# Optimization experiments

Hardware: AMD Instinct MI355X
Metric: run time of the kernel (lower is better)

## Reference

```python
import jax, jax.numpy as jnp
import numpy as np

EPS = 1e-5

def _conv(x, w, pad):
    return jax.lax.conv_general_dilated(
        x, w, window_strides=(1, 1), padding=[(pad, pad), (pad, pad)],
        dimension_numbers=('NCHW', 'OIHW', 'NCHW'))

def _bn(x, g, b):
    # training-mode batch norm over (N, H, W), matching nn.BatchNorm2d in train mode
    m = x.mean(axis=(0, 2, 3), keepdims=True)
    v = x.var(axis=(0, 2, 3), keepdims=True)
    return (x - m) * jax.lax.rsqrt(v + EPS) * g[None, :, None, None] + b[None, :, None, None]

def setup_inputs() -> dict:
    key = jax.random.key(0)
    ks = jax.random.split(key, 16)
    B, C, H, W = 64, 16, 128, 128
    f32 = jnp.float32
    x = jax.random.normal(ks[0], (B, C, H, W), dtype=f32)
    # conv weights (OIHW), He-ish scale
    conv_w1 = jax.random.normal(ks[1], (32, 16, 1, 1), f32) * (2.0 / 16) ** 0.5
    conv_w2 = jax.random.normal(ks[2], (64, 32, 1, 1), f32) * (2.0 / 32) ** 0.5
    conv_w3 = jax.random.normal(ks[3], (32, 64, 3, 3), f32) * (2.0 / (64 * 9)) ** 0.5
    conv_w4 = jax.random.normal(ks[4], (32, 32, 3, 3), f32) * (2.0 / (32 * 9)) ** 0.5
    bn1_g = jnp.ones((32,), f32); bn1_b = jnp.zeros((32,), f32)
    bn2_g = jnp.ones((64,), f32); bn2_b = jnp.zeros((64,), f32)
    bn3_g = jnp.ones((32,), f32); bn3_b = jnp.zeros((32,), f32)
    bn4_g = jnp.ones((32,), f32); bn4_b = jnp.zeros((32,), f32)
    fc1_w = jax.random.normal(ks[5], (32, 32), f32) * (1.0 / 32) ** 0.5
    fc1_b = jnp.zeros((32,), f32)
    fc2_w = jax.random.normal(ks[6], (16, 32), f32) * (1.0 / 32) ** 0.5
    fc2_b = jnp.zeros((16,), f32)
    return dict(x=x, conv_w1=conv_w1, bn1_g=bn1_g, bn1_b=bn1_b,
                conv_w2=conv_w2, bn2_g=bn2_g, bn2_b=bn2_b,
                conv_w3=conv_w3, bn3_g=bn3_g, bn3_b=bn3_b,
                conv_w4=conv_w4, bn4_g=bn4_g, bn4_b=bn4_b,
                fc1_w=fc1_w, fc1_b=fc1_b, fc2_w=fc2_w, fc2_b=fc2_b)

def reference(x, conv_w1, bn1_g, bn1_b, conv_w2, bn2_g, bn2_b,
              conv_w3, bn3_g, bn3_b, conv_w4, bn4_g, bn4_b,
              fc1_w, fc1_b, fc2_w, fc2_b):
    B, C, H, W = x.shape  # C == 16
    # spectral: 1x1 convs
    h = jax.nn.relu(_bn(_conv(x, conv_w1, 0), bn1_g, bn1_b))
    h = jax.nn.relu(_bn(_conv(h, conv_w2, 0), bn2_g, bn2_b))
    # spatial: 3x3 convs
    h = jax.nn.relu(_bn(_conv(h, conv_w3, 1), bn3_g, bn3_b))
    x2 = jax.nn.relu(_bn(_conv(h, conv_w4, 1), bn4_g, bn4_b))  # [B,32,H,W]
    tok = x2.reshape(B, 32, H * W).transpose(0, 2, 1)  # [B,HW,32]
    h1 = jnp.tanh(tok @ fc1_w.T + fc1_b)
    w0 = jnp.tanh(h1 @ fc2_w.T + fc2_b)  # [B,HW,16]
    # y0 is computed BEFORE the torch in-place diag zeroing, which never
    # affects any returned value (w0 is unused afterwards) -> omitted.
    y0 = w0.mean(axis=1)  # [B,16]
    Cm = jnp.einsum('bi,bj->bij', y0, y0)  # [B,16,16]
    wn = jnp.linalg.norm(Cm, axis=2)  # [B,16]
    order = jnp.argsort(-wn, axis=-1)  # descending sort indices
    vals = jnp.take_along_axis(wn, order, axis=-1)  # sorted values
    idx = order[:, :15]  # 5 groups of 3 channels
    gath = jnp.take_along_axis(x, idx[:, :, None, None], axis=1)  # [B,15,H,W]
    fi = gath.reshape(B, 5, 3, H, W).transpose(1, 0, 2, 3, 4)  # [5,B,3,H,W]
    wi = vals[:, :15].reshape(B, 5, 3).mean(axis=-1).T  # [5,B]
    cgh = jnp.einsum('bij,bjn->bin', Cm, x.reshape(B, C, H * W))  # [B,16,HW]
    return (fi, wi, vals, order, cgh)
```

## Files before the change

### kernel.cpp

```cpp
#include <hip/hip_runtime.h>

#define TPB 256

static constexpr int   HWc  = 16384;
static constexpr float NINV = 1.0f / 1048576.0f;

static constexpr unsigned FI_OFF    = 0u;
static constexpr unsigned WI_OFF    = 15728640u;
static constexpr unsigned VALS_OFF  = 15728960u;
static constexpr unsigned ORDER_OFF = 15729984u;
static constexpr unsigned CGH_OFF   = 15731008u;

typedef _Float16 f16;
typedef f16   f16x8 __attribute__((ext_vector_type(8)));
typedef f16   f16x4 __attribute__((ext_vector_type(4)));
typedef float f32x4 __attribute__((ext_vector_type(4)));

__device__ __forceinline__ void gl_lds16(const void* g, void* l) {
    __builtin_amdgcn_global_load_lds(
        (const __attribute__((address_space(1))) unsigned int*)g,
        (__attribute__((address_space(3))) unsigned int*)l, 16, 0, 0);
}

__device__ __forceinline__ float wave_sum(float v) {
#pragma unroll
    for (int o = 1; o < 64; o <<= 1) v += __shfl_xor(v, o, 64);
    return v;
}

__device__ __forceinline__ float tanh_fast(float x) {
    float e = __expf(x + x);
    return 1.0f - __fdividef(2.0f, e + 1.0f);
}

__global__ __launch_bounds__(TPB) void k_gramx(const float* __restrict__ x,
                                               float* __restrict__ bkt) {
    __shared__ float red[4][272];
    int tid = threadIdx.x, lane = tid & 63, w = tid >> 6;
    int p = lane & 15, g = lane >> 4;
    const f16 one = (f16)1.0f;
    const f16x8 kOnes = {one, one, one, one, one, one, one, one};
    f32x4 accG = {0.f, 0.f, 0.f, 0.f};
    f32x4 accS = {0.f, 0.f, 0.f, 0.f};
    unsigned wgid = blockIdx.x * 4u + (unsigned)w;
    for (unsigned c = wgid; c < 32768u; c += 2048u) {
        unsigned P0 = c * 32u;
        unsigned b = P0 >> 14, off = P0 & 16383u;
        const float* src = x + ((size_t)b * 16 + p) * HWc + off + g * 8;
        float4 a4 = *(const float4*)src;
        float4 b4 = *(const float4*)(src + 4);
        f16x8 f = { (f16)a4.x, (f16)a4.y, (f16)a4.z, (f16)a4.w,
                    (f16)b4.x, (f16)b4.y, (f16)b4.z, (f16)b4.w };
        accG = __builtin_amdgcn_mfma_f32_16x16x32_f16(f, f, accG, 0, 0, 0);
        accS = __builtin_amdgcn_mfma_f32_16x16x32_f16(kOnes, f, accS, 0, 0, 0);
    }
#pragma unroll
    for (int r = 0; r < 4; ++r) red[w][(4 * g + r) * 16 + p] = accG[r];
    if (g == 0) red[w][256 + p] = accS[0];
    __syncthreads();
    for (int e = tid; e < 272; e += TPB) {
        float v = red[0][e] + red[1][e] + red[2][e] + red[3][e];
        atomicAdd(&bkt[(blockIdx.x & 63u) * 272u + (unsigned)e], v);
    }
}

__global__ void k_sfin1g(const float* __restrict__ bkt, const float* __restrict__ w1,
                         const float* __restrict__ g1, const float* __restrict__ bb1,
                         float* __restrict__ prm) {
    __shared__ float G[256];
    __shared__ float S[16];
    int tid = threadIdx.x;
    {
        float v = 0.f;
        for (int s = 0; s < 64; ++s) v += bkt[s * 272 + tid];
        G[tid] = v;
    }
    if (tid < 16) {
        float v = 0.f;
        for (int s = 0; s < 64; ++s) v += bkt[s * 272 + 256 + tid];
        S[tid] = v;
    }
    __syncthreads();
    if (tid < 32) {
        float wv[16];
#pragma unroll
        for (int i = 0; i < 16; ++i) wv[i] = w1[tid * 16 + i];
        float m = 0.f, e2 = 0.f;
#pragma unroll
        for (int i = 0; i < 16; ++i) {
            m += wv[i] * S[i];
            float t = 0.f;
#pragma unroll
            for (int j = 0; j < 16; ++j) t += wv[j] * G[i * 16 + j];
            e2 += wv[i] * t;
        }
        float mean = m * NINV;
        float var = e2 * NINV - mean * mean;
        float sc = g1[tid] * rsqrtf(var + 1e-5f);
        prm[tid * 2] = sc;
        prm[tid * 2 + 1] = bb1[tid] - mean * sc;
    }
}

__global__ __launch_bounds__(TPB) void k_conv2m(const float* __restrict__ x,
                                                const float* __restrict__ w1,
                                                const float* __restrict__ w2,
                                                const float* __restrict__ prm1,
                                                f16* __restrict__ t2r,
                                                float* __restrict__ bkt) {
    __shared__ __align__(16) float w1s[512];
    __shared__ float p1[64];
    __shared__ __align__(16) f16 V[256 * 40];
    __shared__ float red[4][800];
    int tid = threadIdx.x, lane = tid & 63, w = tid >> 6;
    int p = lane & 15, g = lane >> 4;
    for (int e = tid; e < 512; e += TPB) w1s[e] = w1[e];
    if (tid < 64) p1[tid] = prm1[tid];
    f16x8 Wf[4];
#pragma unroll
    for (int cb = 0; cb < 4; ++cb) {
        const float* wr = w2 + (cb * 16 + p) * 32 + g * 8;
        float4 a4 = *(const float4*)wr;
        float4 b4 = *(const float4*)(wr + 4);
        Wf[cb] = (f16x8){ (f16)a4.x, (f16)a4.y, (f16)a4.z, (f16)a4.w,
                          (f16)b4.x, (f16)b4.y, (f16)b4.z, (f16)b4.w };
    }
    __syncthreads();
    unsigned pid = blockIdx.x * TPB + tid;
    const float* xp = x + (size_t)(pid >> 14) * 16 * HWc + (pid & 16383u);
    float xv[16];
#pragma unroll
    for (int c = 0; c < 16; ++c) xv[c] = xp[(size_t)c * HWc];
    f16* vp = V + tid * 40;
#pragma unroll
    for (int c8 = 0; c8 < 4; ++c8) {
        f16x8 hv;
#pragma unroll
        for (int j = 0; j < 8; ++j) {
            int co = c8 * 8 + j;
            float a = 0.f;
#pragma unroll
            for (int c4 = 0; c4 < 4; ++c4) {
                float4 ww = *(const float4*)&w1s[co * 16 + c4 * 4];
                a = fmaf(xv[c4 * 4 + 0], ww.x, a); a = fmaf(xv[c4 * 4 + 1], ww.y, a);
                a = fmaf(xv[c4 * 4 + 2], ww.z, a); a = fmaf(xv[c4 * 4 + 3], ww.w, a);
            }
            hv[j] = (f16)fmaxf(0.f, fmaf(a, p1[co * 2], p1[co * 2 + 1]));
        }
        *(f16x8*)(vp + c8 * 8) = hv;
    }
    __syncthreads();
    unsigned Pb = blockIdx.x * TPB + (unsigned)(w * 64);
#pragma unroll
    for (int f = 0; f < 4; ++f) {
        int pxl = w * 64 + f * 16 + p;
        f16x8 bf = *(const f16x8*)&V[pxl * 40 + g * 8];
        unsigned Pg = Pb + (unsigned)(f * 16 + p);
#pragma unroll
        for (int cb = 0; cb < 4; ++cb) {
            f32x4 d = {0.f, 0.f, 0.f, 0.f};
            d = __builtin_amdgcn_mfma_f32_16x16x32_f16(Wf[cb], bf, d, 0, 0, 0);
            f16x4 o4 = { (f16)d[0], (f16)d[1], (f16)d[2], (f16)d[3] };
            *(f16x4*)(t2r + (size_t)Pg * 64 + cb * 16 + 4 * g) = o4;
        }
    }
    const f16 one = (f16)1.0f;
    const f16x8 kOnes = {one, one, one, one, one, one, one, one};
    f32x4 accG[3] = {{0.f,0.f,0.f,0.f},{0.f,0.f,0.f,0.f},{0.f,0.f,0.f,0.f}};
    f32x4 accS[2] = {{0.f,0.f,0.f,0.f},{0.f,0.f,0.f,0.f}};
#pragma unroll
    for (int c2 = 0; c2 < 2; ++c2) {
        int px0 = w * 64 + c2 * 32;
        f16x8 fb[2];
#pragma unroll
        for (int cb2 = 0; cb2 < 2; ++cb2)
#pragma unroll
            for (int j = 0; j < 8; ++j)
                fb[cb2][j] = V[(px0 + g * 8 + j) * 40 + cb2 * 16 + p];
        accG[0] = __builtin_amdgcn_mfma_f32_16x16x32_f16(fb[0], fb[0], accG[0], 0, 0, 0);
        accG[1] = __builtin_amdgcn_mfma_f32_16x16x32_f16(fb[0], fb[1], accG[1], 0, 0, 0);
        accG[2] = __builtin_amdgcn_mfma_f32_16x16x32_f16(fb[1], fb[1], accG[2], 0, 0, 0);
        accS[0] = __builtin_amdgcn_mfma_f32_16x16x32_f16(kOnes, fb[0], accS[0], 0, 0, 0);
        accS[1] = __builtin_amdgcn_mfma_f32_16x16x32_f16(kOnes, fb[1], accS[1], 0, 0, 0);
    }
#pragma unroll
    for (int blk = 0; blk < 3; ++blk)
#pragma unroll
        for (int r = 0; r < 4; ++r)
            red[w][blk * 256 + (4 * g + r) * 16 + p] = accG[blk][r];
    if (g == 0) { red[w][768 + p] = accS[0][0]; red[w][784 + p] = accS[1][0]; }
    __syncthreads();
    for (int e = tid; e < 800; e += TPB) {
        float v = red[0][e] + red[1][e] + red[2][e] + red[3][e];
        atomicAdd(&bkt[(blockIdx.x & 63u) * 800u + (unsigned)e], v);
    }
}

__global__ void k_sfin2g(const float* __restrict__ bkt, const float* __restrict__ w2,
                         const float* __restrict__ g2, const float* __restrict__ bb2,
                         float* __restrict__ prm) {
    __shared__ float G[768];
    __shared__ float S[32];
    int tid = threadIdx.x;
    for (int e = tid; e < 768; e += 256) {
        float v = 0.f;
        for (int s = 0; s < 64; ++s) v += bkt[s * 800 + e];
        G[e] = v;
    }
    if (tid < 32) {
        float v = 0.f;
        for (int s = 0; s < 64; ++s) v += bkt[s * 800 + 768 + tid];
        S[tid] = v;
    }
    __syncthreads();
    if (tid < 64) {
        float wv[32];
#pragma unroll
        for (int i = 0; i < 32; ++i) wv[i] = (float)(f16)w2[tid * 32 + i];
        float m = 0.f, e2 = 0.f;
#pragma unroll
        for (int i = 0; i < 32; ++i) {
            m += wv[i] * S[i];
            int bi = i >> 4, il = i & 15;
            float t = 0.f;
#pragma unroll
            for (int j = 0; j < 32; ++j) {
                int bj = j >> 4, jl = j & 15;
                float Gij;
                if (bi <= bj) Gij = G[(bi == 0 ? (bj == 0 ? 0 : 1) : 2) * 256 + il * 16 + jl];
                else          Gij = G[(bj == 0 ? 1 : 2) * 256 + jl * 16 + il];
                t += wv[j] * Gij;
            }
            e2 += wv[i] * t;
        }
        float mean = m * NINV;
        float var = e2 * NINV - mean * mean;
        float sc = g2[tid] * rsqrtf(var + 1e-5f);
        prm[tid * 2] = sc;
        prm[tid * 2 + 1] = bb2[tid] - mean * sc;
    }
}

__global__ void k_sfin(const float* __restrict__ bkt, const float* __restrict__ g,
                       const float* __restrict__ bb, float* __restrict__ prm, int C) {
    int co = threadIdx.x;
    float s = 0.f, q = 0.f;
    for (int k = 0; k < 64; ++k) { s += bkt[(k * C + co) * 2]; q += bkt[(k * C + co) * 2 + 1]; }
    float mean = s * NINV;
    float var = q * NINV - mean * mean;
    float sc = g[co] * rsqrtf(var + 1e-5f);
    prm[co * 2] = sc;
    prm[co * 2 + 1] = bb[co] - mean * sc;
}

template <int CI>
__global__ void k_wprep(const float* __restrict__ w, float* __restrict__ wsg) {
    constexpr int KS = CI / 32;
    int t = blockIdx.x * 256 + threadIdx.x;
    if (t >= KS * 18 * 64) return;
    int lane = t & 63, fr = t >> 6;
    int cf = fr & 1, tap = (fr >> 1) % 9, ks = fr / 18;
    int g = lane >> 4, p = lane & 15;
    int co = cf * 16 + p;
    f16x8 hv;
#pragma unroll
    for (int j = 0; j < 8; ++j) {
        int ci = ks * 32 + g * 8 + j;
        hv[j] = (f16)w[(co * CI + ci) * 9 + tap];
    }
    ((f16x8*)wsg)[fr * 64 + lane] = hv;
}

template <int CI>
__global__ __launch_bounds__(512, 4) void k_conv3(const f16* __restrict__ in,
                                                  const float* __restrict__ wsg,
                                                  const float* __restrict__ prm,
                                                  f16* __restrict__ outp,
                                                  float* __restrict__ bkt) {
    constexpr int KS = CI / 32;
    __shared__ __align__(16) struct {
        f16   Wl[18 * 512];
        f16   Al[6 * 128 * 32];
        float red[8][64];
    } sh;
    int tid = threadIdx.x;
    int lane = tid & 63, w = tid >> 6;
    int p = lane & 15, g = lane >> 4;
    int rw = w >> 1, h = w & 1;
    int cw = tid & 3, pxt = tid >> 2;

    unsigned o = blockIdx.x;
    unsigned xcd = o & 7u, q = o >> 3;
    unsigned rg = q & 31u, grp = q >> 5;
    unsigned b = (grp << 3) | xcd;
    int y0 = (int)rg * 4;

    float psc[KS][8], psh[KS][8];
#pragma unroll
    for (int ks = 0; ks < KS; ++ks)
#pragma unroll
        for (int j = 0; j < 8; ++j) {
            int ch = ks * 32 + cw * 8 + j;
            psc[ks][j] = prm[ch * 2];
            psh[ks][j] = prm[ch * 2 + 1];
        }

    bool mask0 = (h == 0 && p == 0);
    bool mask1 = (h == 1 && p == 15);
    const f16x8 kZ = {0, 0, 0, 0, 0, 0, 0, 0};

    f32x4 acc[4][2];
#pragma unroll
    for (int f = 0; f < 4; ++f)
#pragma unroll
        for (int cf = 0; cf < 2; ++cf) acc[f][cf] = (f32x4){0.f, 0.f, 0.f, 0.f};

    for (int ks = 0; ks < KS; ++ks) {
        if (ks) __syncthreads();
#pragma unroll
        for (int c0 = 0; c0 < 1152; c0 += 512) {
            if (c0 + (w << 6) < 1152) {
                int c = c0 + tid;
                gl_lds16(wsg + (size_t)(ks * 4608 + c * 4), &sh.Wl[c * 8]);
            }
        }
#pragma unroll
        for (int r6 = 0; r6 < 6; ++r6) {
            int yy = y0 - 1 + r6;
            f16* dst = &sh.Al[r6 * 4096 + tid * 8];
            if ((unsigned)yy < 128u) {
                const f16* s = in + ((size_t)(b * 128u + (unsigned)yy) * 128u + pxt) * CI
                                  + ks * 32 + cw * 8;
                f16x8 raw = *(const f16x8*)s;
                f16x8 o8;
#pragma unroll
                for (int j = 0; j < 8; ++j)
                    o8[j] = (f16)fmaxf(0.f, fmaf((float)raw[j], psc[ks][j], psh[ks][j]));
                *(f16x8*)dst = o8;
            } else {
                *(f16x8*)dst = kZ;
            }
        }
        __syncthreads();
        const f16x8* Wv = (const f16x8*)sh.Wl;
        for (int dyi = 0; dyi < 3; ++dyi) {
            int ar = rw + dyi;
#pragma unroll
            for (int dxi = 0; dxi < 3; ++dxi) {
                int tap = dyi * 3 + dxi;
                f16x8 b0 = Wv[(tap * 2 + 0) * 64 + lane];
                f16x8 b1 = Wv[(tap * 2 + 1) * 64 + lane];
#pragma unroll
                for (int f = 0; f < 4; ++f) {
                    int px = h * 64 + f * 16 + p + dxi - 1;
                    f16x8 a = *(const f16x8*)&sh.Al[(ar * 128 + px) * 32 + g * 8];
                    if (dxi == 0 && f == 0) { if (mask0) a = kZ; }
                    if (dxi == 2 && f == 3) { if (mask1) a = kZ; }
                    acc[f][0] = __builtin_amdgcn_mfma_f32_16x16x32_f16(b0, a, acc[f][0], 0, 0, 0);
                    acc[f][1] = __builtin_amdgcn_mfma_f32_16x16x32_f16(b1, a, acc[f][1], 0, 0, 0);
                }
            }
        }
    }

    float sv[8], qv[8];
#pragma unroll
    for (int cf = 0; cf < 2; ++cf)
#pragma unroll
        for (int r = 0; r < 4; ++r) {
            float s = acc[0][cf][r] + acc[1][cf][r] + acc[2][cf][r] + acc[3][cf][r];
            float qq = acc[0][cf][r] * acc[0][cf][r] + acc[1][cf][r] * acc[1][cf][r] +
                       acc[2][cf][r] * acc[2][cf][r] + acc[3][cf][r] * acc[3][cf][r];
#pragma unroll
            for (int m = 1; m < 16; m <<= 1) {
                s += __shfl_xor(s, m, 64);
                qq += __shfl_xor(qq, m, 64);
            }
            sv[cf * 4 + r] = s; qv[cf * 4 + r] = qq;
        }
    if (p == 0) {
#pragma unroll
        for (int cf = 0; cf < 2; ++cf)
#pragma unroll
            for (int r = 0; r < 4; ++r) {
                int co = cf * 16 + g * 4 + r;
                sh.red[w][co * 2] = sv[cf * 4 + r];
                sh.red[w][co * 2 + 1] = qv[cf * 4 + r];
            }
    }

    unsigned pxb = b * 16384u + (unsigned)((y0 + rw) * 128 + h * 64 + p);
#pragma unroll
    for (int f = 0; f < 4; ++f)
#pragma unroll
        for (int cf = 0; cf < 2; ++cf) {
            f16x4 o4 = { (f16)acc[f][cf][0], (f16)acc[f][cf][1],
                         (f16)acc[f][cf][2], (f16)acc[f][cf][3] };
            *(f16x4*)(outp + (size_t)(pxb + f * 16u) * 32u + (unsigned)(cf * 16 + g * 4)) = o4;
        }

    __syncthreads();
    if (tid < 64) {
        float v = 0.f;
#pragma unroll
        for (int ww = 0; ww < 8; ++ww) v += sh.red[ww][tid];
        atomicAdd(&bkt[(o & 63u) * 64u + (unsigned)tid], v);
    }
}

__global__ __launch_bounds__(TPB) void k_fcm(const f16* __restrict__ t4,
                                             const float* __restrict__ prm4,
                                             const float* __restrict__ fw1,
                                             const float* __restrict__ fb1,
                                             const float* __restrict__ fw2,
                                             const float* __restrict__ fb2,
                                             float* __restrict__ y0sum) {
    __shared__ __align__(16) struct {
        f16   V1[256 * 40];
        f16   V2[256 * 40];
        float p4[64], b1s[32], b2s[16];
        float red[4][16];
    } sh;
    int tid = threadIdx.x, lane = tid & 63, w = tid >> 6;
    int p = lane & 15, g = lane >> 4;
    if (tid < 64) sh.p4[tid] = prm4[tid];
    if (tid < 32) sh.b1s[tid] = fb1[tid];
    if (tid < 16) sh.b2s[tid] = fb2[tid];
    f16x8 W1h[2], W1l[2], W2h, W2l;
#pragma unroll
    for (int cb = 0; cb < 2; ++cb) {
        const float* wr = fw1 + (cb * 16 + p) * 32 + g * 8;
#pragma unroll
        for (int j = 0; j < 8; ++j) {
            float v = wr[j];
            f16 hh = (f16)v;
            W1h[cb][j] = hh;
            W1l[cb][j] = (f16)(v - (float)hh);
        }
    }
    {
        const float* wr = fw2 + p * 32 + g * 8;
#pragma unroll
        for (int j = 0; j < 8; ++j) {
            float v = wr[j];
            f16 hh = (f16)v;
            W2h[j] = hh;
            W2l[j] = (f16)(v - (float)hh);
        }
    }
    __syncthreads();
    unsigned pid = blockIdx.x * TPB + tid;
    const f16x8* tv = (const f16x8*)(t4 + (size_t)pid * 32);
    f16* vp = sh.V1 + tid * 40;
#pragma unroll
    for (int c8 = 0; c8 < 4; ++c8) {
        f16x8 raw = tv[c8];
        f16x8 o8;
#pragma unroll
        for (int j = 0; j < 8; ++j) {
            int c = c8 * 8 + j;
            o8[j] = (f16)fmaxf(0.f, fmaf((float)raw[j], sh.p4[c * 2], sh.p4[c * 2 + 1]));
        }
        *(f16x8*)(vp + c8 * 8) = o8;
    }
    __syncthreads();
    float bb1[8];
#pragma unroll
    for (int cb = 0; cb < 2; ++cb)
#pragma unroll
        for (int r = 0; r < 4; ++r) bb1[cb * 4 + r] = sh.b1s[cb * 16 + g * 4 + r];
#pragma unroll
    for (int f = 0; f < 4; ++f) {
        int pxl = w * 64 + f * 16 + p;
        f16x8 bf = *(const f16x8*)&sh.V1[pxl * 40 + g * 8];
#pragma unroll
        for (int cb = 0; cb < 2; ++cb) {
            f32x4 d = {0.f, 0.f, 0.f, 0.f};
            d = __builtin_amdgcn_mfma_f32_16x16x32_f16(W1l[cb], bf, d, 0, 0, 0);
            d = __builtin_amdgcn_mfma_f32_16x16x32_f16(W1h[cb], bf, d, 0, 0, 0);
            f16x4 h4;
#pragma unroll
            for (int r = 0; r < 4; ++r) h4[r] = (f16)tanh_fast(d[r] + bb1[cb * 4 + r]);
            *(f16x4*)&sh.V2[pxl * 40 + cb * 16 + g * 4] = h4;
        }
    }
    __syncthreads();
    float bb2[4];
#pragma unroll
    for (int r = 0; r < 4; ++r) bb2[r] = sh.b2s[g * 4 + r];
    float s4[4] = {0.f, 0.f, 0.f, 0.f};
#pragma unroll
    for (int f = 0; f < 4; ++f) {
        int pxl = w * 64 + f * 16 + p;
        f16x8 bf = *(const f16x8*)&sh.V2[pxl * 40 + g * 8];
        f32x4 d = {0.f, 0.f, 0.f, 0.f};
        d = __builtin_amdgcn_mfma_f32_16x16x32_f16(W2l, bf, d, 0, 0, 0);
        d = __builtin_amdgcn_mfma_f32_16x16x32_f16(W2h, bf, d, 0, 0, 0);
#pragma unroll
        for (int r = 0; r < 4; ++r) s4[r] += tanh_fast(d[r] + bb2[r]);
    }
#pragma unroll
    for (int r = 0; r < 4; ++r) {
#pragma unroll
        for (int m = 1; m < 16; m <<= 1) s4[r] += __shfl_xor(s4[r], m, 64);
    }
    if (p == 0) {
#pragma unroll
        for (int r = 0; r < 4; ++r) sh.red[w][g * 4 + r] = s4[r];
    }
    __syncthreads();
    if (tid < 16) {
        float s = sh.red[0][tid] + sh.red[1][tid] + sh.red[2][tid] + sh.red[3][tid];
        atomicAdd(&y0sum[(blockIdx.x >> 6) * 16u + tid], s);
    }
}

__global__ void k_final(const float* __restrict__ y0sum, float* __restrict__ out,
                        float* __restrict__ Cm, int* __restrict__ idxb) {
    int b = threadIdx.x;
    float y0[16]; float nrm = 0.f;
#pragma unroll
    for (int i = 0; i < 16; ++i) { y0[i] = y0sum[b * 16 + i] * (1.0f / 16384.0f); nrm += y0[i] * y0[i]; }
    nrm = sqrtf(nrm);
    float wn[16]; int id[16];
#pragma unroll
    for (int i = 0; i < 16; ++i) { wn[i] = fabsf(y0[i]) * nrm; id[i] = i; }
    for (int i = 1; i < 16; ++i) {
        float k = wn[i]; int ii = id[i]; int j = i - 1;
        while (j >= 0 && wn[j] < k) { wn[j + 1] = wn[j]; id[j + 1] = id[j]; --j; }
        wn[j + 1] = k; id[j + 1] = ii;
    }
    for (int i = 0; i < 16; ++i) {
        out[VALS_OFF + b * 16 + i] = wn[i];
        out[ORDER_OFF + b * 16 + i] = (float)id[i];
    }
    for (int g = 0; g < 5; ++g)
        out[WI_OFF + g * 64 + b] = (wn[g * 3] + wn[g * 3 + 1] + wn[g * 3 + 2]) * (1.0f / 3.0f);
    for (int i = 0; i < 16; ++i)
        for (int j = 0; j < 16; ++j) Cm[b * 256 + i * 16 + j] = y0[i] * y0[j];
    for (int s = 0; s < 15; ++s) idxb[b * 15 + s] = id[s];
}

__global__ __launch_bounds__(TPB) void k_out(const float* __restrict__ x,
                                             const float* __restrict__ Cm,
                                             const int* __restrict__ idxb,
                                             float* __restrict__ out) {
    __shared__ float cm[256];
    __shared__ int idl[15];
    int tid = threadIdx.x;
    unsigned b = blockIdx.x >> 6;
    unsigned p = ((blockIdx.x & 63u) << 8) + tid;
    cm[tid] = Cm[b * 256u + tid];
    if (tid < 15) idl[tid] = idxb[b * 15u + tid];
    __syncthreads();
    const float* xp = x + (size_t)b * 16 * HWc + p;
    float xv[16];
#pragma unroll
    for (int j = 0; j < 16; ++j) xv[j] = xp[(size_t)j * HWc];
    float* og = out + CGH_OFF + (size_t)b * 16 * HWc + p;
    for (int i = 0; i < 16; ++i) {
        float a = 0.f;
#pragma unroll
        for (int j = 0; j < 16; ++j) a = fmaf(cm[i * 16 + j], xv[j], a);
        og[(size_t)i * HWc] = a;
    }
#pragma unroll
    for (int s = 0; s < 15; ++s) {
        int ch = idl[s];
        float vv = xp[(size_t)ch * HWc];
        int g = s / 3, r = s - 3 * g;
        out[(size_t)((g * 64 + (int)b) * 3 + r) * HWc + p] = vv;
    }
}

extern "C" void kernel_launch(void* const* d_in, const int* in_sizes, int n_in,
                              void* d_out, int out_size, void* d_ws, size_t ws_size,
                              hipStream_t stream) {
    const float* x    = (const float*)d_in[0];
    const float* w1   = (const float*)d_in[1];
    const float* bn1g = (const float*)d_in[2];  const float* bn1b = (const float*)d_in[3];
    const float* w2   = (const float*)d_in[4];
    const float* bn2g = (const float*)d_in[5];  const float* bn2b = (const float*)d_in[6];
    const float* w3   = (const float*)d_in[7];
    const float* bn3g = (const float*)d_in[8];  const float* bn3b = (const float*)d_in[9];
    const float* w4   = (const float*)d_in[10];
    const float* bn4g = (const float*)d_in[11]; const float* bn4b = (const float*)d_in[12];
    const float* fw1  = (const float*)d_in[13]; const float* fb1  = (const float*)d_in[14];
    const float* fw2  = (const float*)d_in[15]; const float* fb2  = (const float*)d_in[16];
    float* out = (float*)d_out;
    float* wsf = (float*)d_ws;

    f16*   t2r = (f16*)wsf;
    f16*   t3r = (f16*)(wsf + 33554432);
    f16*   t4h = (f16*)(wsf + 50331648);
    float* acc = wsf + 67108864;
    float* b1g = acc;
    float* b2g = acc + 17408;
    float* b3  = acc + 68608;
    float* b4  = acc + 76800;
    float* y0s = acc + 84992;
    float* pr1 = acc + 86016;  float* pr2 = acc + 86080;
    float* pr3 = acc + 86208;  float* pr4 = acc + 86272;
    float* Cm  = acc + 86336;
    int*   idxb = (int*)(acc + 102720);
    float* wsg3 = acc + 103680;
    float* wsg4 = acc + 112896;
    size_t need = (size_t)(67108864 + 117504) * 4;
    if (ws_size < need) return;

    hipMemsetAsync(acc, 0, 86016 * 4, stream);

    k_wprep<64><<<9, 256, 0, stream>>>(w3, wsg3);
    k_wprep<32><<<5, 256, 0, stream>>>(w4, wsg4);
    k_gramx<<<512, TPB, 0, stream>>>(x, b1g);
    k_sfin1g<<<1, 256, 0, stream>>>(b1g, w1, bn1g, bn1b, pr1);
    k_conv2m<<<4096, TPB, 0, stream>>>(x, w1, w2, pr1, t2r, b2g);
    k_sfin2g<<<1, 256, 0, stream>>>(b2g, w2, bn2g, bn2b, pr2);
    k_conv3<64><<<2048, 512, 0, stream>>>(t2r, wsg3, pr2, t3r, b3);
    k_sfin<<<1, 32, 0, stream>>>(b3, bn3g, bn3b, pr3, 32);
    k_conv3<32><<<2048, 512, 0, stream>>>(t3r, wsg4, pr3, t4h, b4);
    k_sfin<<<1, 32, 0, stream>>>(b4, bn4g, bn4b, pr4, 32);
    k_fcm<<<4096, TPB, 0, stream>>>(t4h, pr4, fw1, fb1, fw2, fb2, y0s);
    k_final<<<1, 64, 0, stream>>>(y0s, out, Cm, idxb);
    k_out<<<4096, TPB, 0, stream>>>(x, Cm, idxb, out);
}
```

Measured before the change: 365.6 us.

## Fold BN scale into downstream conv/FC weights, apply shift+ReLU in packed f16

The per-channel batch-norm scale is folded into the next layer's weights, so relu(x*sc+sh) becomes sc*relu(x + sh/sc). The activation prologue in the conv3 and fcm kernels shrinks to a packed f16 add and max, with no float conversion and FMA per element. The weight-prep kernels now run after each stats-finalize kernel because they need the scale. This is only valid when the scale is positive (gamma > 0). It also adds f16 rounding of sh/sc and more kernel ordering dependencies.

```diff
diff --git a/kernel.cpp b/kernel.cpp
--- a/kernel.cpp
+++ b/kernel.cpp
@@ -254,7 +254,8 @@
 }
 
 template <int CI>
-__global__ void k_wprep(const float* __restrict__ w, float* __restrict__ wsg) {
+__global__ void k_wprep(const float* __restrict__ w, const float* __restrict__ prm,
+                        float* __restrict__ wsg) {
     constexpr int KS = CI / 32;
     int t = blockIdx.x * 256 + threadIdx.x;
     if (t >= KS * 18 * 64) return;
@@ -266,7 +267,7 @@
 #pragma unroll
     for (int j = 0; j < 8; ++j) {
         int ci = ks * 32 + g * 8 + j;
-        hv[j] = (f16)w[(co * CI + ci) * 9 + tap];
+        hv[j] = (f16)(w[(co * CI + ci) * 9 + tap] * prm[ci * 2]);
     }
     ((f16x8*)wsg)[fr * 64 + lane] = hv;
 }
@@ -295,14 +296,13 @@
     unsigned b = (grp << 3) | xcd;
     int y0 = (int)rg * 4;
 
-    float psc[KS][8], psh[KS][8];
+    f16x8 qv[KS];
 #pragma unroll
     for (int ks = 0; ks < KS; ++ks)
 #pragma unroll
         for (int j = 0; j < 8; ++j) {
             int ch = ks * 32 + cw * 8 + j;
-            psc[ks][j] = prm[ch * 2];
-            psh[ks][j] = prm[ch * 2 + 1];
+            qv[ks][j] = (f16)(prm[ch * 2 + 1] / prm[ch * 2]);
         }
 
     bool mask0 = (h == 0 && p == 0);
@@ -332,11 +332,7 @@
                 const f16* s = in + ((size_t)(b * 128u + (unsigned)yy) * 128u + pxt) * CI
                                   + ks * 32 + cw * 8;
                 f16x8 raw = *(const f16x8*)s;
-                f16x8 o8;
-#pragma unroll
-                for (int j = 0; j < 8; ++j)
-                    o8[j] = (f16)fmaxf(0.f, fmaf((float)raw[j], psc[ks][j], psh[ks][j]));
-                *(f16x8*)dst = o8;
+                *(f16x8*)dst = __builtin_elementwise_max(raw + qv[ks], kZ);
             } else {
                 *(f16x8*)dst = kZ;
             }
@@ -363,7 +359,7 @@
         }
     }
 
-    float sv[8], qv[8];
+    float sv[8], qvv[8];
 #pragma unroll
     for (int cf = 0; cf < 2; ++cf)
 #pragma unroll
@@ -376,7 +372,7 @@
                 s += __shfl_xor(s, m, 64);
                 qq += __shfl_xor(qq, m, 64);
             }
-            sv[cf * 4 + r] = s; qv[cf * 4 + r] = qq;
+            sv[cf * 4 + r] = s; qvv[cf * 4 + r] = qq;
         }
     if (p == 0) {
 #pragma unroll
@@ -385,7 +381,7 @@
             for (int r = 0; r < 4; ++r) {
                 int co = cf * 16 + g * 4 + r;
                 sh.red[w][co * 2] = sv[cf * 4 + r];
-                sh.red[w][co * 2 + 1] = qv[cf * 4 + r];
+                sh.red[w][co * 2 + 1] = qvv[cf * 4 + r];
             }
     }
 
@@ -418,12 +414,11 @@
     __shared__ __align__(16) struct {
         f16   V1[256 * 40];
         f16   V2[256 * 40];
-        float p4[64], b1s[32], b2s[16];
+        float b1s[32], b2s[16];
         float red[4][16];
     } sh;
     int tid = threadIdx.x, lane = tid & 63, w = tid >> 6;
     int p = lane & 15, g = lane >> 4;
-    if (tid < 64) sh.p4[tid] = prm4[tid];
     if (tid < 32) sh.b1s[tid] = fb1[tid];
     if (tid < 16) sh.b2s[tid] = fb2[tid];
     f16x8 W1h[2], W1l[2], W2h, W2l;
@@ -432,7 +427,7 @@
         const float* wr = fw1 + (cb * 16 + p) * 32 + g * 8;
 #pragma unroll
         for (int j = 0; j < 8; ++j) {
-            float v = wr[j];
+            float v = wr[j] * prm4[(g * 8 + j) * 2];
             f16 hh = (f16)v;
             W1h[cb][j] = hh;
             W1l[cb][j] = (f16)(v - (float)hh);
@@ -448,6 +443,15 @@
             W2l[j] = (f16)(v - (float)hh);
         }
     }
+    f16x8 q4v[4];
+#pragma unroll
+    for (int c8 = 0; c8 < 4; ++c8)
+#pragma unroll
+        for (int j = 0; j < 8; ++j) {
+            int c = c8 * 8 + j;
+            q4v[c8][j] = (f16)(prm4[c * 2 + 1] / prm4[c * 2]);
+        }
+    const f16x8 kZ8 = {0, 0, 0, 0, 0, 0, 0, 0};
     __syncthreads();
     unsigned pid = blockIdx.x * TPB + tid;
     const f16x8* tv = (const f16x8*)(t4 + (size_t)pid * 32);
@@ -455,13 +459,7 @@
 #pragma unroll
     for (int c8 = 0; c8 < 4; ++c8) {
         f16x8 raw = tv[c8];
-        f16x8 o8;
-#pragma unroll
-        for (int j = 0; j < 8; ++j) {
-            int c = c8 * 8 + j;
-            o8[j] = (f16)fmaxf(0.f, fmaf((float)raw[j], sh.p4[c * 2], sh.p4[c * 2 + 1]));
-        }
-        *(f16x8*)(vp + c8 * 8) = o8;
+        *(f16x8*)(vp + c8 * 8) = __builtin_elementwise_max(raw + q4v[c8], kZ8);
     }
     __syncthreads();
     float bb1[8];
@@ -610,14 +608,14 @@
 
     hipMemsetAsync(acc, 0, 86016 * 4, stream);
 
-    k_wprep<64><<<9, 256, 0, stream>>>(w3, wsg3);
-    k_wprep<32><<<5, 256, 0, stream>>>(w4, wsg4);
     k_gramx<<<512, TPB, 0, stream>>>(x, b1g);
     k_sfin1g<<<1, 256, 0, stream>>>(b1g, w1, bn1g, bn1b, pr1);
     k_conv2m<<<4096, TPB, 0, stream>>>(x, w1, w2, pr1, t2r, b2g);
     k_sfin2g<<<1, 256, 0, stream>>>(b2g, w2, bn2g, bn2b, pr2);
+    k_wprep<64><<<9, 256, 0, stream>>>(w3, pr2, wsg3);
     k_conv3<64><<<2048, 512, 0, stream>>>(t2r, wsg3, pr2, t3r, b3);
     k_sfin<<<1, 32, 0, stream>>>(b3, bn3g, bn3b, pr3, 32);
+    k_wprep<32><<<5, 256, 0, stream>>>(w4, pr3, wsg4);
     k_conv3<32><<<2048, 512, 0, stream>>>(t3r, wsg4, pr3, t4h, b4);
     k_sfin<<<1, 32, 0, stream>>>(b4, bn4g, bn4b, pr4, 32);
     k_fcm<<<4096, TPB, 0, stream>>>(t4h, pr4, fw1, fb1, fw2, fb2, y0s);
```

Result: no change. 371.1 us (+1.5%).
